# Performance work log

Measured on AMD Instinct MI355X. Metric: run time of the kernel, lower is better.

The kernel has to match this reference:

```python
import jax, jax.numpy as jnp
import numpy as np

B, S, E, C, H = 64, 2048, 512, 512, 256


def setup_inputs() -> dict:
    key = jax.random.key(0)
    ks = jax.random.split(key, 8)
    encoder_word_embeds = jax.random.normal(ks[0], (B, S, E), dtype=jnp.float32)
    encoder_lengths = jax.random.randint(ks[1], (B,), 1, S + 1)  # lengths in [1, S]
    context_state = jax.random.normal(ks[2], (B, C), dtype=jnp.float32)
    # Learned parameters (nn.Linear style: y = x @ W.T + b)
    sw = 1.0 / np.sqrt(E)
    sc = 1.0 / np.sqrt(C)
    sh = 1.0 / np.sqrt(H)
    W_word = jax.random.uniform(ks[3], (H, E), minval=-sw, maxval=sw, dtype=jnp.float32)
    b_word = jax.random.uniform(ks[4], (H,), minval=-sw, maxval=sw, dtype=jnp.float32)
    W_ctx = jax.random.uniform(ks[5], (H, C), minval=-sc, maxval=sc, dtype=jnp.float32)
    b_ctx = jax.random.uniform(ks[6], (H,), minval=-sc, maxval=sc, dtype=jnp.float32)
    w_hidden = jax.random.uniform(ks[7], (H,), minval=-sh, maxval=sh, dtype=jnp.float32)  # hidden_layer has no bias
    return {
        "encoder_word_embeds": encoder_word_embeds,
        "encoder_lengths": encoder_lengths,
        "context_state": context_state,
        "W_word": W_word,
        "b_word": b_word,
        "W_ctx": W_ctx,
        "b_ctx": b_ctx,
        "w_hidden": w_hidden,
    }


def reference(encoder_word_embeds, encoder_lengths, context_state, W_word, b_word, W_ctx, b_ctx, w_hidden):
    seq_len = encoder_word_embeds.shape[1]
    # word mask [B, S]: positions < length
    positions = jnp.arange(seq_len)  # [S]
    mask = (positions[None, :] < encoder_lengths[:, None]).astype(jnp.float32)  # [B, S]
    # additive attention MLP
    word_feat = jnp.einsum("bse,he->bsh", encoder_word_embeds, W_word) + b_word  # [B,S,H]
    ctx_feat = context_state @ W_ctx.T + b_ctx  # [B,H]
    scores = jnp.einsum("bsh,h->bs", jnp.tanh(word_feat + ctx_feat[:, None, :]), w_hidden)  # [B,S]
    # softmax over seq, then mask and renormalize (matches original order)
    attn = jax.nn.softmax(scores, axis=1) * mask
    attn = attn / (1e-10 + attn.sum(axis=1, keepdims=True))  # [B,S]
    attention_features = jnp.einsum("bs,bse->be", attn, encoder_word_embeds)  # [B,E]
    return attention_features, attn
```

## Files before the change

kernel.cpp:

```cpp
#include <hip/hip_runtime.h>
#include <hip/hip_bf16.h>
#include <cstdint>
#include <cstddef>

#define B_  64
#define S_  2048
#define E_  512
#define C_  512
#define H_  256

using f32x4 = __attribute__((ext_vector_type(4))) float;
using s16x8 = __attribute__((ext_vector_type(8))) short;

__device__ __forceinline__ uint2 f4_to_bf4(float4 v) {
    __hip_bfloat162 lo = __float22bfloat162_rn(make_float2(v.x, v.y));
    __hip_bfloat162 hi = __float22bfloat162_rn(make_float2(v.z, v.w));
    union { __hip_bfloat162 b; unsigned u; } a, c;
    a.b = lo; c.b = hi;
    return make_uint2(a.u, c.u);
}

__device__ __forceinline__ void async16(const void* g, void* l) {
    __builtin_amdgcn_global_load_lds(
        (const __attribute__((address_space(1))) void*)g,
        (__attribute__((address_space(3))) void*)l,
        16, 0, 0);
}

__global__ void prep_kernel(const float* __restrict__ W, unsigned short* __restrict__ Wb,
                            const float* __restrict__ ctx, const float* __restrict__ Wc,
                            const float* __restrict__ bc, const float* __restrict__ bw,
                            float* __restrict__ cb) {
    __shared__ float row[C_];
    int blk = blockIdx.x, t = threadIdx.x;
    if (blk < 128) {
        int i = (blk * 256 + t) * 4;
        float4 v = *(const float4*)(W + i);
        *(uint2*)(Wb + i) = f4_to_bf4(v);
    } else {
        int b = blk - 128;
        row[t] = ctx[b * C_ + t];
        row[t + 256] = ctx[b * C_ + t + 256];
        __syncthreads();
        const float4* w4 = (const float4*)(Wc + (size_t)t * C_);
        const float4* x4 = (const float4*)row;
        float acc = 0.f;
        #pragma unroll 4
        for (int c = 0; c < C_ / 4; ++c) {
            float4 w = w4[c], x = x4[c];
            acc += w.x * x.x + w.y * x.y + w.z * x.z + w.w * x.w;
        }
        cb[b * H_ + t] = acc + bc[t] + bw[t];
    }
}

#define BM 128
#define BN 256
#define BK 64
#define LDT 72

__global__ __launch_bounds__(512) void scores_kernel(
    const float* __restrict__ A,
    const unsigned short* __restrict__ Wb,
    const float* __restrict__ cb,
    const float* __restrict__ wh,
    const int*   __restrict__ lens,
    float* __restrict__ scores,
    float* __restrict__ Wpart,
    float* __restrict__ mtpart)
{
    __shared__ __align__(16) unsigned short At[BM * LDT];
    __shared__ __align__(16) unsigned short Bt[BN * 64];
    __shared__ float sblk[BM];
    __shared__ float pblk[BM];
    int t = threadIdx.x;
    int m0 = blockIdx.x * BM;
    int b  = m0 >> 11;
    int ms = m0 & (S_ - 1);
    int len = lens[b];
    if (ms >= len) return;

    int w = t >> 6, lane = t & 63, quad = lane >> 4, lm = lane & 15;
    int wm = (w & 1) * 64, wn = (w >> 1) * 64;

    if (t < BM) sblk[t] = 0.f;

    f32x4 acc[4][4] = {};

    int arow = t >> 4, acol = (t & 15) * 4;
    int la8 = lane >> 3, lc8 = lane & 7;

    for (int k0 = 0; k0 < E_; k0 += BK) {
        #pragma unroll
        for (int j = 0; j < 4; ++j) {
            int r  = (w << 5) + (j << 3) + la8;
            int cg = (lc8 ^ (r & 7)) << 3;
            async16(Wb + (size_t)r * E_ + k0 + cg,
                    (char*)Bt + (((w << 5) + (j << 3)) << 7));
        }
        #pragma unroll
        for (int i = 0; i < 4; ++i) {
            int r = arow + i * 32;
            float4 v = *(const float4*)(A + (size_t)(m0 + r) * E_ + k0 + acol);
            *(uint2*)(At + r * LDT + acol) = f4_to_bf4(v);
        }
        __syncthreads();
        #pragma unroll
        for (int ks = 0; ks < 2; ++ks) {
            s16x8 af[4], bfr[4];
            #pragma unroll
            for (int i = 0; i < 4; ++i)
                af[i] = *(const s16x8*)(At + (wm + i * 16 + lm) * LDT + ks * 32 + quad * 8);
            #pragma unroll
            for (int i = 0; i < 4; ++i) {
                int r = wn + i * 16 + lm;
                int c = (ks * 4 + quad) ^ (r & 7);
                bfr[i] = *(const s16x8*)(Bt + r * 64 + c * 8);
            }
            #pragma unroll
            for (int mi = 0; mi < 4; ++mi)
                #pragma unroll
                for (int ni = 0; ni < 4; ++ni)
                    acc[mi][ni] = __builtin_amdgcn_mfma_f32_16x16x32_bf16(
                        af[mi], bfr[ni], acc[mi][ni], 0, 0, 0);
        }
        __syncthreads();
    }

    float wv[4], cbv[4];
    #pragma unroll
    for (int ni = 0; ni < 4; ++ni) {
        int n = wn + ni * 16 + lm;
        wv[ni]  = wh[n];
        cbv[ni] = cb[b * H_ + n];
    }
    #pragma unroll
    for (int mi = 0; mi < 4; ++mi) {
        #pragma unroll
        for (int r = 0; r < 4; ++r) {
            float p = 0.f;
            #pragma unroll
            for (int ni = 0; ni < 4; ++ni) {
                float x = acc[mi][ni][r] + cbv[ni];
                x = fminf(fmaxf(x, -15.f), 15.f);
                float e = __expf(2.f * x);
                float th = 1.f - 2.f * __builtin_amdgcn_rcpf(e + 1.f);
                p += wv[ni] * th;
            }
            #pragma unroll
            for (int off = 8; off >= 1; off >>= 1)
                p += __shfl_xor(p, off);
            if (lm == 0)
                atomicAdd(&sblk[wm + mi * 16 + quad * 4 + r], p);
        }
    }
    __syncthreads();
    if (t < BM) scores[m0 + t] = sblk[t];

    int nvalid = len - ms; if (nvalid > BM) nvalid = BM;
    float m_l = -1e30f;
    #pragma unroll 16
    for (int r = 0; r < BM; ++r) {
        float sv = (r < nvalid) ? sblk[r] : -1e30f;
        m_l = fmaxf(m_l, sv);
    }
    if (t < BM) pblk[t] = (t < nvalid) ? __expf(sblk[t] - m_l) : 0.f;
    __syncthreads();
    float t_l = 0.f;
    #pragma unroll 16
    for (int r = 0; r < BM; ++r) t_l += pblk[r];
    float accw = 0.f;
    const float* ab = A + (size_t)m0 * E_ + t;
    #pragma unroll 8
    for (int r = 0; r < BM; ++r)
        accw += pblk[r] * ab[(size_t)r * E_];
    Wpart[(size_t)blockIdx.x * E_ + t] = accw;
    if (t == 0) {
        mtpart[blockIdx.x * 2 + 0] = m_l;
        mtpart[blockIdx.x * 2 + 1] = t_l;
    }
}

__global__ __launch_bounds__(512) void finalize_kernel(
    const int* __restrict__ lens, const float* __restrict__ Wpart,
    const float* __restrict__ mtpart,
    float* __restrict__ attn,
    float* __restrict__ feat)
{
    int b = blockIdx.x, t = threadIdx.x;
    int len = lens[b];
    int L = (len + BM - 1) / BM;
    int base = b * (S_ / BM);
    float M = -1e30f;
    for (int l = 0; l < L; ++l) M = fmaxf(M, mtpart[(base + l) * 2]);
    float T = 0.f;
    for (int l = 0; l < L; ++l)
        T += __expf(mtpart[(base + l) * 2] - M) * mtpart[(base + l) * 2 + 1];
    float inv = 1.f / T;
    float acc = 0.f;
    for (int l = 0; l < L; ++l)
        acc += __expf(mtpart[(base + l) * 2] - M) * Wpart[(size_t)(base + l) * E_ + t];
    feat[b * E_ + t] = acc * inv;
    float* sc = attn + (size_t)b * S_;
    #pragma unroll
    for (int i = 0; i < 4; ++i) {
        int s = t + i * 512;
        float v = sc[s];
        sc[s] = (s < len) ? __expf(v - M) * inv : 0.f;
    }
}

extern "C" void kernel_launch(void* const* d_in, const int* in_sizes, int n_in,
                              void* d_out, int out_size, void* d_ws, size_t ws_size,
                              hipStream_t stream) {
    const float* embeds = (const float*)d_in[0];
    const int*   lens   = (const int*)d_in[1];
    const float* ctx    = (const float*)d_in[2];
    const float* Ww     = (const float*)d_in[3];
    const float* bw     = (const float*)d_in[4];
    const float* Wc     = (const float*)d_in[5];
    const float* bc     = (const float*)d_in[6];
    const float* wh     = (const float*)d_in[7];
    float* out  = (float*)d_out;
    float* feat = out;
    float* attn = out + B_ * E_;

    char* ws = (char*)d_ws;
    unsigned short* Wb = (unsigned short*)ws;
    float* cb     = (float*)(ws + 256 * 1024);
    float* Wpart  = (float*)(ws + 320 * 1024);
    float* mtpart = (float*)(ws + 320 * 1024 + 2 * 1024 * 1024);

    prep_kernel<<<192, 256, 0, stream>>>(Ww, Wb, ctx, Wc, bc, bw, cb);
    scores_kernel<<<dim3(B_ * S_ / BM), 512, 0, stream>>>(embeds, Wb, cb, wh, lens,
                                                          attn, Wpart, mtpart);
    finalize_kernel<<<B_, 512, 0, stream>>>(lens, Wpart, mtpart, attn, feat);
}
```

Before: 418.9 us.

## Double-buffer GEMM tiles and use warp-shuffle reductions for block softmax stats

The scores kernel's K loop now uses two LDS buffers: the next tile's W async loads and A global loads are issued before the MFMAs on the current tile, and the A bf16 conversion store happens afterward. This halves the barriers per step and hides global latency behind compute. The block max and sum over 128 scores move from serial per-thread loops to wavefront shuffle reductions. LDS use roughly doubles, which may lower occupancy, and more registers are live to hold the prefetched A values.

Result: slower. 434.3 us (+3.7%).

```diff
diff --git a/kernel.cpp b/kernel.cpp
--- a/kernel.cpp
+++ b/kernel.cpp
@@ -69,10 +69,11 @@
     float* __restrict__ Wpart,
     float* __restrict__ mtpart)
 {
-    __shared__ __align__(16) unsigned short At[BM * LDT];
-    __shared__ __align__(16) unsigned short Bt[BN * 64];
+    __shared__ __align__(16) unsigned short At[2][BM * LDT];
+    __shared__ __align__(16) unsigned short Bt[2][BN * 64];
     __shared__ float sblk[BM];
     __shared__ float pblk[BM];
+    __shared__ float wred[2], wredt[2];
     int t = threadIdx.x;
     int m0 = blockIdx.x * BM;
     int b  = m0 >> 11;
@@ -90,32 +91,52 @@
     int arow = t >> 4, acol = (t & 15) * 4;
     int la8 = lane >> 3, lc8 = lane & 7;
 
-    for (int k0 = 0; k0 < E_; k0 += BK) {
-        #pragma unroll
-        for (int j = 0; j < 4; ++j) {
-            int r  = (w << 5) + (j << 3) + la8;
-            int cg = (lc8 ^ (r & 7)) << 3;
-            async16(Wb + (size_t)r * E_ + k0 + cg,
-                    (char*)Bt + (((w << 5) + (j << 3)) << 7));
-        }
-        #pragma unroll
-        for (int i = 0; i < 4; ++i) {
-            int r = arow + i * 32;
-            float4 v = *(const float4*)(A + (size_t)(m0 + r) * E_ + k0 + acol);
-            *(uint2*)(At + r * LDT + acol) = f4_to_bf4(v);
-        }
-        __syncthreads();
+    #pragma unroll
+    for (int j = 0; j < 4; ++j) {
+        int r  = (w << 5) + (j << 3) + la8;
+        int cg = (lc8 ^ (r & 7)) << 3;
+        async16(Wb + (size_t)r * E_ + cg,
+                (char*)Bt[0] + (((w << 5) + (j << 3)) << 7));
+    }
+    {
+        float4 av[4];
+        #pragma unroll
+        for (int i = 0; i < 4; ++i)
+            av[i] = *(const float4*)(A + (size_t)(m0 + arow + i * 32) * E_ + acol);
+        #pragma unroll
+        for (int i = 0; i < 4; ++i)
+            *(uint2*)(At[0] + (arow + i * 32) * LDT + acol) = f4_to_bf4(av[i]);
+    }
+    __syncthreads();
+
+    int cur = 0;
+    for (int step = 0; step < 8; ++step) {
+        int nxt = cur ^ 1;
+        int k1 = (step + 1) * BK;
+        float4 av[4];
+        if (step < 7) {
+            #pragma unroll
+            for (int j = 0; j < 4; ++j) {
+                int r  = (w << 5) + (j << 3) + la8;
+                int cg = (lc8 ^ (r & 7)) << 3;
+                async16(Wb + (size_t)r * E_ + k1 + cg,
+                        (char*)Bt[nxt] + (((w << 5) + (j << 3)) << 7));
+            }
+            #pragma unroll
+            for (int i = 0; i < 4; ++i)
+                av[i] = *(const float4*)(A + (size_t)(m0 + arow + i * 32) * E_ + k1 + acol);
+        }
         #pragma unroll
         for (int ks = 0; ks < 2; ++ks) {
             s16x8 af[4], bfr[4];
             #pragma unroll
             for (int i = 0; i < 4; ++i)
-                af[i] = *(const s16x8*)(At + (wm + i * 16 + lm) * LDT + ks * 32 + quad * 8);
+                af[i] = *(const s16x8*)(At[cur] + (wm + i * 16 + lm) * LDT + ks * 32 + quad * 8);
             #pragma unroll
             for (int i = 0; i < 4; ++i) {
                 int r = wn + i * 16 + lm;
                 int c = (ks * 4 + quad) ^ (r & 7);
-                bfr[i] = *(const s16x8*)(Bt + r * 64 + c * 8);
+                bfr[i] = *(const s16x8*)(Bt[cur] + r * 64 + c * 8);
             }
             #pragma unroll
             for (int mi = 0; mi < 4; ++mi)
@@ -124,7 +145,13 @@
                     acc[mi][ni] = __builtin_amdgcn_mfma_f32_16x16x32_bf16(
                         af[mi], bfr[ni], acc[mi][ni], 0, 0, 0);
         }
+        if (step < 7) {
+            #pragma unroll
+            for (int i = 0; i < 4; ++i)
+                *(uint2*)(At[nxt] + (arow + i * 32) * LDT + acol) = f4_to_bf4(av[i]);
+        }
         __syncthreads();
+        cur = nxt;
     }
 
     float wv[4], cbv[4];
@@ -158,17 +185,23 @@
     if (t < BM) scores[m0 + t] = sblk[t];
 
     int nvalid = len - ms; if (nvalid > BM) nvalid = BM;
-    float m_l = -1e30f;
-    #pragma unroll 16
-    for (int r = 0; r < BM; ++r) {
-        float sv = (r < nvalid) ? sblk[r] : -1e30f;
-        m_l = fmaxf(m_l, sv);
-    }
-    if (t < BM) pblk[t] = (t < nvalid) ? __expf(sblk[t] - m_l) : 0.f;
-    __syncthreads();
-    float t_l = 0.f;
-    #pragma unroll 16
-    for (int r = 0; r < BM; ++r) t_l += pblk[r];
+    if (t < 128) {
+        float v = (t < nvalid) ? sblk[t] : -1e30f;
+        float mm = v;
+        #pragma unroll
+        for (int off = 32; off >= 1; off >>= 1) mm = fmaxf(mm, __shfl_xor(mm, off));
+        if ((t & 63) == 0) wred[t >> 6] = mm;
+    }
+    __syncthreads();
+    float m_l = fmaxf(wred[0], wred[1]);
+    if (t < 128) {
+        float p = (t < nvalid) ? __expf(sblk[t] - m_l) : 0.f;
+        pblk[t] = p;
+        #pragma unroll
+        for (int off = 32; off >= 1; off >>= 1) p += __shfl_xor(p, off);
+        if ((t & 63) == 0) wredt[t >> 6] = p;
+    }
+    __syncthreads();
     float accw = 0.f;
     const float* ab = A + (size_t)m0 * E_ + t;
     #pragma unroll 8
@@ -177,7 +210,7 @@
     Wpart[(size_t)blockIdx.x * E_ + t] = accw;
     if (t == 0) {
         mtpart[blockIdx.x * 2 + 0] = m_l;
-        mtpart[blockIdx.x * 2 + 1] = t_l;
+        mtpart[blockIdx.x * 2 + 1] = wredt[0] + wredt[1];
     }
 }
 
```
